# Optimization experiments

Measured on AMD Instinct MI355X. Metric: run time of the kernel, lower is better.

## Reference

```python
import jax, jax.numpy as jnp
import numpy as np

B, T, D, H = 8, 256, 1024, 512
NUM_SPANS = T * (T + 1) // 2          # triangular span enumeration
K = int(2.0 * T)                      # pruning_ratio * num_tokens
NUM_GOLD = 10
NEG = -1e20                           # allennlp replace_masked_values fill

# static triangular (start, end) index tables: for start in range(T): for end in range(start, T)
_starts = np.repeat(np.arange(T), np.arange(T, 0, -1))
_ends = np.concatenate([np.arange(s, T) for s in range(T)])
START_IDX = jnp.asarray(_starts, dtype=jnp.int32)
END_IDX = jnp.asarray(_ends, dtype=jnp.int32)


def setup_inputs() -> dict:
    key = jax.random.key(0)
    ks = jax.random.split(key, 8)
    inputs = jax.random.normal(ks[0], (B, T, D), dtype=jnp.float32)
    input_mask = jnp.ones((B, T), dtype=jnp.int32)
    # gold spans with start <= end, all in range (sorted along last dim)
    answer_spans = jnp.sort(jax.random.randint(ks[1], (B, NUM_GOLD, 2), 0, T), axis=-1)
    sD = 1.0 / np.sqrt(D)
    sH = 1.0 / np.sqrt(H)
    W_start = jax.random.uniform(ks[2], (D, H), jnp.float32, -sD, sD)
    b_start = jax.random.uniform(ks[3], (H,), jnp.float32, -sD, sD)
    W_end = jax.random.uniform(ks[4], (D, H), jnp.float32, -sD, sD)
    b_end = jax.random.uniform(ks[5], (H,), jnp.float32, -sD, sD)
    w_score = jax.random.uniform(ks[6], (H, 1), jnp.float32, -sH, sH)
    b_score = jax.random.uniform(ks[7], (1,), jnp.float32, -sH, sH)
    return {"inputs": inputs, "input_mask": input_mask, "answer_spans": answer_spans,
            "W_start": W_start, "b_start": b_start, "W_end": W_end, "b_end": b_end,
            "w_score": w_score, "b_score": b_score}


def reference(inputs, input_mask, answer_spans, W_start, b_start, W_end, b_end, w_score, b_score):
    # SpanRepAssembly: project starts/ends, pairwise-sum over triangular spans
    hs = inputs @ W_start + b_start                        # [B,T,H]
    he = inputs @ W_end + b_end                            # [B,T,H]
    span_hidden = hs[:, START_IDX, :] + he[:, END_IDX, :]  # [B,S,H]
    m = input_mask.astype(bool)
    span_mask = m[:, START_IDX] & m[:, END_IDX]            # [B,S]

    # span scorer: ReLU -> Linear(H,1)
    scores = jax.nn.relu(span_hidden) @ w_score + b_score  # [B,S,1]
    scores = jnp.where(span_mask[..., None], scores, NEG)

    # Pruner: top-k by score, indices sorted ascending, gather
    _, top_idx = jax.lax.top_k(scores[..., 0], K)          # [B,K]
    top_idx = jnp.sort(top_idx, axis=1)
    top_logits = jnp.take_along_axis(scores, top_idx[..., None], axis=1)       # [B,K,1]
    top_mask = jnp.take_along_axis(span_mask, top_idx, axis=1)[..., None].astype(jnp.float32)
    top_probs = jax.nn.sigmoid(top_logits) * top_mask

    # gold prediction map (union policy): labels[b, tri_index(span)] = 1
    s0 = answer_spans[..., 0].astype(jnp.int32)
    e0 = answer_spans[..., 1].astype(jnp.int32)
    gmask = (s0 >= 0)
    arg_idx = (2 * s0 * T - s0 * s0 + s0) // 2 + (e0 - s0)
    arg_idx = jnp.where(gmask, arg_idx, 0)
    labels = jnp.zeros((B, NUM_SPANS), jnp.float32)
    labels = labels.at[jnp.arange(B)[:, None], arg_idx].max(gmask.astype(jnp.float32))
    pred = jnp.take_along_axis(labels[..., None], top_idx[..., None], axis=1)  # [B,K,1]

    # BCE-with-logits, weight=top_mask, reduction='sum' (stable form)
    l = top_logits
    bce = jnp.maximum(l, 0.0) - l * pred + jnp.log1p(jnp.exp(-jnp.abs(l)))
    loss = jnp.sum(top_mask * bce)
    return top_probs, loss
```

## Files before the change

kernel.cpp:

```cpp
#include <hip/hip_runtime.h>
#include <hip/hip_bf16.h>
#include <math.h>

#define BB 8
#define TT 256
#define DD 1024
#define HH 512
#define NSPANS 32896
#define KK 512
#define NEGV -1e20f
#define NCH 32
#define CHSZ 1028
#define NT16 72

typedef __attribute__((ext_vector_type(8))) short bf16x8;
typedef __attribute__((ext_vector_type(4))) float f32x4;

__device__ inline unsigned short f2bf(float f) {
    unsigned u = __float_as_uint(f);
    return (unsigned short)((u + 0x7FFFu + ((u >> 16) & 1u)) >> 16);
}
__device__ inline float bf2f(unsigned short u) {
    return __uint_as_float(((unsigned)u) << 16);
}
__device__ inline void split3(float v, unsigned short& a, unsigned short& b,
                              unsigned short& c) {
    a = f2bf(v);           float r  = v - bf2f(a);
    b = f2bf(r);           float r2 = r - bf2f(b);
    c = f2bf(r2);
}

__global__ __launch_bounds__(256) void prep(
    const float* __restrict__ X,
    const float* __restrict__ Ws, const float* __restrict__ We,
    unsigned short* __restrict__ x0, unsigned short* __restrict__ x1,
    unsigned short* __restrict__ x2, unsigned short* __restrict__ wt,
    unsigned* __restrict__ zp)
{
    const int blk = blockIdx.x;
    const int tid = threadIdx.x;

    if (blk < 2048) {
        const int i4 = blk * 256 + tid;
        const float4 v = ((const float4*)X)[i4];
        const float vv[4] = {v.x, v.y, v.z, v.w};
        ushort4 h0, h1, h2;
        unsigned short* p0 = (unsigned short*)&h0;
        unsigned short* p1 = (unsigned short*)&h1;
        unsigned short* p2 = (unsigned short*)&h2;
        #pragma unroll
        for (int j = 0; j < 4; ++j) split3(vv[j], p0[j], p1[j], p2[j]);
        ((ushort4*)x0)[i4] = h0;
        ((ushort4*)x1)[i4] = h1;
        ((ushort4*)x2)[i4] = h2;
    } else if (blk < 3072) {
        __shared__ float lt[32][33];
        const int blk2 = blk - 2048;
        const int z   = blk2 >> 9;
        const int rem = blk2 & 511;
        const int k0  = (rem >> 4) * 32;
        const int h0  = (rem & 15) * 32;

        const float* Wz = z ? We : Ws;
        {
            const int row = tid >> 3, c4 = tid & 7;
            const float4 v = *(const float4*)&Wz[(k0 + row) * HH + h0 + c4 * 4];
            lt[row][c4*4 + 0] = v.x;
            lt[row][c4*4 + 1] = v.y;
            lt[row][c4*4 + 2] = v.z;
            lt[row][c4*4 + 3] = v.w;
        }
        __syncthreads();
        {
            const int n = h0 + (tid >> 3), kq = tid & 7;
            ushort4 o0, o1, o2;
            unsigned short* q0 = (unsigned short*)&o0;
            unsigned short* q1 = (unsigned short*)&o1;
            unsigned short* q2 = (unsigned short*)&o2;
            #pragma unroll
            for (int u = 0; u < 4; ++u)
                split3(lt[kq*4 + u][tid >> 3], q0[u], q1[u], q2[u]);
            unsigned short* base = wt + (size_t)z * 3 * 524288;
            const int off = n * 1024 + k0 + kq * 4;
            *(ushort4*)&base[0 * 524288 + off] = o0;
            *(ushort4*)&base[1 * 524288 + off] = o1;
            *(ushort4*)&base[2 * 524288 + off] = o2;
        }
    } else {
        const int i = (blk - 3072) * 256 + tid;
        for (int k = i; k < 32777; k += 32 * 256) zp[k] = 0u;
    }
}

__global__ __launch_bounds__(256) void gemm_mfma(
    const unsigned short* __restrict__ xs,
    const unsigned short* __restrict__ wt,
    const float* __restrict__ bs, const float* __restrict__ be,
    float* __restrict__ hs, float* __restrict__ he)
{
    const int bid = blockIdx.x;
    const int lg  = ((bid & 7) << 6) + (bid >> 3);
    const int z   = lg >> 8;
    const int my  = (lg & 255) >> 3, nx = lg & 7;
    const int m0 = my * 64, n0 = nx * 64;

    const unsigned short* __restrict__ W = wt + (size_t)z * 3 * 524288;
    const float* __restrict__ bias = z ? be : bs;
    float* __restrict__ Y = z ? he : hs;

    __shared__ __align__(16) unsigned short la[3][64][72];
    __shared__ __align__(16) unsigned short lb[3][64][72];

    const int tid = threadIdx.x;
    const int wave = tid >> 6, lane = tid & 63;
    const int wm = (wave >> 1) * 32, wn = (wave & 1) * 32;

    f32x4 acc[2][2];
    #pragma unroll
    for (int i = 0; i < 2; ++i)
        #pragma unroll
        for (int j = 0; j < 2; ++j) acc[i][j] = (f32x4){0.f, 0.f, 0.f, 0.f};

    const int rA = lane & 15;
    const int kq = lane >> 4;

    for (int kt = 0; kt < 16; ++kt) {
        const int k0 = kt * 64;
        __syncthreads();
        #pragma unroll
        for (int sp = 0; sp < 3; ++sp) {
            #pragma unroll
            for (int it = 0; it < 2; ++it) {
                const int idx = it * 256 + tid;
                const int row = idx >> 3, c8 = idx & 7;
                *(int4*)&la[sp][row][c8 * 8] =
                    *(const int4*)&xs[(size_t)sp * 2097152 + (m0 + row) * 1024 + k0 + c8 * 8];
                *(int4*)&lb[sp][row][c8 * 8] =
                    *(const int4*)&W[(size_t)sp * 524288 + (n0 + row) * 1024 + k0 + c8 * 8];
            }
        }
        __syncthreads();

        #pragma unroll
        for (int s = 0; s < 2; ++s) {
            const int kl = s * 32 + kq * 8;
            bf16x8 af[3][2], bg[3][2];
            #pragma unroll
            for (int sp = 0; sp < 3; ++sp) {
                #pragma unroll
                for (int f = 0; f < 2; ++f) {
                    af[sp][f] = *(const bf16x8*)&la[sp][wm + f * 16 + rA][kl];
                    bg[sp][f] = *(const bf16x8*)&lb[sp][wn + f * 16 + rA][kl];
                }
            }
            #pragma unroll
            for (int fm = 0; fm < 2; ++fm)
                #pragma unroll
                for (int fn = 0; fn < 2; ++fn) {
                    acc[fm][fn] = __builtin_amdgcn_mfma_f32_16x16x32_bf16(
                        af[0][fm], bg[0][fn], acc[fm][fn], 0, 0, 0);
                    acc[fm][fn] = __builtin_amdgcn_mfma_f32_16x16x32_bf16(
                        af[0][fm], bg[1][fn], acc[fm][fn], 0, 0, 0);
                    acc[fm][fn] = __builtin_amdgcn_mfma_f32_16x16x32_bf16(
                        af[1][fm], bg[0][fn], acc[fm][fn], 0, 0, 0);
                    acc[fm][fn] = __builtin_amdgcn_mfma_f32_16x16x32_bf16(
                        af[1][fm], bg[1][fn], acc[fm][fn], 0, 0, 0);
                    acc[fm][fn] = __builtin_amdgcn_mfma_f32_16x16x32_bf16(
                        af[0][fm], bg[2][fn], acc[fm][fn], 0, 0, 0);
                    acc[fm][fn] = __builtin_amdgcn_mfma_f32_16x16x32_bf16(
                        af[2][fm], bg[0][fn], acc[fm][fn], 0, 0, 0);
                }
        }
    }

    const int col = lane & 15, rq = lane >> 4;
    #pragma unroll
    for (int fm = 0; fm < 2; ++fm)
        #pragma unroll
        for (int fn = 0; fn < 2; ++fn) {
            const int nn = n0 + wn + fn * 16 + col;
            const float bv = bias[nn];
            #pragma unroll
            for (int r = 0; r < 4; ++r) {
                const int mm = m0 + wm + fm * 16 + rq * 4 + r;
                Y[mm * HH + nn] = acc[fm][fn][r] + bv;
            }
        }
}

__device__ inline unsigned f2key(float f) {
    unsigned u = __float_as_uint(f);
    return u ^ ((u & 0x80000000u) ? 0xFFFFFFFFu : 0x80000000u);
}

__global__ __launch_bounds__(128) void span_scores(
    const float* __restrict__ hs, const float* __restrict__ he,
    const float* __restrict__ w_score, const float* __restrict__ b_score,
    const int* __restrict__ input_mask, float* __restrict__ scores,
    unsigned* __restrict__ hist12)
{
    const int bx = blockIdx.x;
    const int b = bx / NT16;
    int tI = bx - b * NT16;
    int i = 0, cnt = 8;
    while (tI >= cnt) { tI -= cnt; ++i; cnt = 8 - (i >> 1); }
    const int j = (i >> 1) + tI;
    const int s0 = i * 16, e0 = j * 32;

    __shared__ __align__(16) float shs[16][132];
    __shared__ __align__(16) float she[32][132];
    __shared__ __align__(16) float swc[128];
    __shared__ unsigned lh[2048];

    const int tid = threadIdx.x;
    const float4* hs4 = (const float4*)hs;
    const float4* he4 = (const float4*)he;

    for (int idx = tid; idx < 2048; idx += 128) lh[idx] = 0;

    const int ii = tid >> 4, jj = tid & 15;

    float4 acc[2][2];
    #pragma unroll
    for (int p = 0; p < 2; ++p)
        #pragma unroll
        for (int q = 0; q < 2; ++q) acc[p][q] = make_float4(0.f, 0.f, 0.f, 0.f);

    for (int ck = 0; ck < 4; ++ck) {
        const int kc = ck * 128;
        __syncthreads();
        #pragma unroll
        for (int l = 0; l < 12; ++l) {
            const int idx = l * 128 + tid;
            const int row = idx >> 5, c4 = idx & 31;
            if (row < 16) {
                *(float4*)&shs[row][c4 * 4] =
                    hs4[((b*TT + s0 + row) * HH + kc) / 4 + c4];
            } else {
                *(float4*)&she[row - 16][c4 * 4] =
                    he4[((b*TT + e0 + row - 16) * HH + kc) / 4 + c4];
            }
        }
        if (tid < 32) *(float4*)&swc[tid * 4] =
            ((const float4*)w_score)[kc / 4 + tid];
        __syncthreads();

        #pragma unroll 4
        for (int c4 = 0; c4 < 32; ++c4) {
            const float4 w  = *(const float4*)&swc[c4 * 4];
            const float4 a0 = *(const float4*)&shs[ii][c4 * 4];
            const float4 a1 = *(const float4*)&shs[ii + 8][c4 * 4];
            const float4 v0 = *(const float4*)&she[jj][c4 * 4];
            const float4 v1 = *(const float4*)&she[jj + 16][c4 * 4];
            #pragma unroll
            for (int p = 0; p < 2; ++p) {
                const float4 a = p ? a1 : a0;
                #pragma unroll
                for (int q = 0; q < 2; ++q) {
                    const float4 v = q ? v1 : v0;
                    acc[p][q].x += fmaxf(a.x + v.x, 0.f) * w.x;
                    acc[p][q].y += fmaxf(a.y + v.y, 0.f) * w.y;
                    acc[p][q].z += fmaxf(a.z + v.z, 0.f) * w.z;
                    acc[p][q].w += fmaxf(a.w + v.w, 0.f) * w.w;
                }
            }
        }
    }

    const float bsc = b_score[0];
    #pragma unroll
    for (int p = 0; p < 2; ++p) {
        const int s = s0 + ii + p * 8;
        #pragma unroll
        for (int q = 0; q < 2; ++q) {
            const int e = e0 + jj + q * 16;
            if (e >= s) {
                const float4 a4 = acc[p][q];
                float scv = (a4.x + a4.y) + (a4.z + a4.w) + bsc;
                if (!(input_mask[b*TT + s] && input_mask[b*TT + e])) scv = NEGV;
                scores[b*NSPANS + s*TT - (s*(s-1))/2 + (e - s)] = scv;
                const unsigned bin = f2key(scv) >> 20;
                atomicAdd(&lh[bin >> 1], 1u << ((bin & 1u) * 16));
            }
        }
    }
    __syncthreads();

    for (int idx = tid; idx < 2048; idx += 128) {
        const unsigned w = lh[idx];
        const unsigned lo = w & 0xFFFFu, hi = w >> 16;
        if (lo) atomicAdd(&hist12[b*4096 + 2*idx],     lo);
        if (hi) atomicAdd(&hist12[b*4096 + 2*idx + 1], hi);
    }
}

__global__ __launch_bounds__(256) void findcompact(
    const float* __restrict__ scores, const unsigned* __restrict__ hist12,
    unsigned* __restrict__ thrInfo,
    unsigned* __restrict__ cand, unsigned* __restrict__ candCnt)
{
    const int b = blockIdx.x >> 5, ch = blockIdx.x & 31;
    const unsigned* h = hist12 + b * 4096;
    const int tid = threadIdx.x;
    const int lane = tid & 63, wave = tid >> 6;

    const int topbin = 4095 - tid * 16;
    unsigned psum = 0;
    #pragma unroll
    for (int j = 0; j < 16; ++j) psum += h[topbin - j];

    unsigned inc = psum;
    #pragma unroll
    for (int off = 1; off < 64; off <<= 1) {
        unsigned v = __shfl_up(inc, off);
        if (lane >= off) inc += v;
    }
    __shared__ unsigned wsum4[4], wpre4[4];
    __shared__ unsigned shp[2];
    if (lane == 63) wsum4[wave] = inc;
    __syncthreads();
    if (tid == 0) { unsigned c = 0; for (int w = 0; w < 4; ++w) { wpre4[w] = c; c += wsum4[w]; } }
    __syncthreads();

    const unsigned before = wpre4[wave] + inc - psum;
    if (before < KK && before + psum >= KK) {
        unsigned cum = before;
        int bin = topbin;
        #pragma unroll
        for (int j = 0; j < 16; ++j) {
            const unsigned c = h[topbin - j];
            if (cum + c >= KK) { bin = topbin - j; break; }
            cum += c;
        }
        shp[0] = (unsigned)bin;
        shp[1] = KK - cum;
        thrInfo[b*4 + 0] = (unsigned)bin;
        thrInfo[b*4 + 1] = KK - cum;
    }
    __syncthreads();
    const unsigned p12 = shp[0];

    const float* sc = scores + b * NSPANS;
    const int base = ch * CHSZ;
    for (int i = base + tid; i < base + CHSZ; i += 256) {
        const unsigned key = f2key(sc[i]);
        if ((key >> 20) == p12) {
            const unsigned pos = atomicAdd(&candCnt[b], 1u);
            cand[b*NSPANS + pos] = key & 0xFFFFFu;
        }
    }
}

__global__ __launch_bounds__(1024) void refine(
    const unsigned* __restrict__ cand, const unsigned* __restrict__ candCnt,
    const float* __restrict__ scores,
    unsigned* __restrict__ thrInfo, unsigned* __restrict__ chunkBase)
{
    const int b = blockIdx.x;
    const unsigned* cd = cand + b*NSPANS;
    const unsigned n = candCnt[b];
    const unsigned remaining = thrInfo[b*4 + 1];
    const int tid = threadIdx.x;
    const int lane = tid & 63, wave = tid >> 6;

    __shared__ unsigned hist[1024];
    __shared__ unsigned wsum[16], wpre[16];
    __shared__ unsigned sh[2], shT[2];

    hist[tid] = 0;
    __syncthreads();
    for (unsigned i = tid; i < n; i += 1024) atomicAdd(&hist[(cd[i] >> 10) & 1023u], 1u);
    __syncthreads();
    {
        const unsigned psum = hist[1023 - tid];
        unsigned inc = psum;
        #pragma unroll
        for (int off = 1; off < 64; off <<= 1) {
            unsigned v = __shfl_up(inc, off);
            if (lane >= off) inc += v;
        }
        if (lane == 63) wsum[wave] = inc;
        __syncthreads();
        if (tid == 0) { unsigned c = 0; for (int w = 0; w < 16; ++w) { wpre[w] = c; c += wsum[w]; } }
        __syncthreads();
        const unsigned before = wpre[wave] + inc - psum;
        if (before < remaining && before + psum >= remaining && psum > 0) {
            sh[0] = 1023u - (unsigned)tid;
            sh[1] = remaining - before;
        }
        __syncthreads();
    }
    const unsigned b1 = sh[0], rem1 = sh[1];
    __syncthreads();

    hist[tid] = 0;
    __syncthreads();
    for (unsigned i = tid; i < n; i += 1024) {
        const unsigned v = cd[i];
        if (((v >> 10) & 1023u) == b1) atomicAdd(&hist[v & 1023u], 1u);
    }
    __syncthreads();
    {
        const unsigned psum = hist[1023 - tid];
        unsigned inc = psum;
        #pragma unroll
        for (int off = 1; off < 64; off <<= 1) {
            unsigned v = __shfl_up(inc, off);
            if (lane >= off) inc += v;
        }
        if (lane == 63) wsum[wave] = inc;
        __syncthreads();
        if (tid == 0) { unsigned c = 0; for (int w = 0; w < 16; ++w) { wpre[w] = c; c += wsum[w]; } }
        __syncthreads();
        const unsigned before = wpre[wave] + inc - psum;
        if (before < rem1 && before + psum >= rem1 && psum > 0) {
            const unsigned thrv = (thrInfo[b*4 + 0] << 20) | (b1 << 10) | (1023u - (unsigned)tid);
            thrInfo[b*4 + 2] = thrv;
            thrInfo[b*4 + 3] = rem1 - before;
            shT[0] = thrv;
            shT[1] = rem1 - before;
        }
    }
    __syncthreads();
    const unsigned thr = shT[0], ties = shT[1];

    __shared__ unsigned cg[NCH], ce[NCH];
    const float* sc = scores + b*NSPANS;
    #pragma unroll
    for (int q = 0; q < 2; ++q) {
        const int ch = wave*2 + q;
        const int base = ch*CHSZ, end = base + CHSZ;
        unsigned g = 0, e = 0;
        for (int i = base + lane; i < end; i += 64) {
            const unsigned key = f2key(sc[i]);
            g += (key > thr); e += (key == thr);
        }
        #pragma unroll
        for (int off = 32; off; off >>= 1) { g += __shfl_down(g, off); e += __shfl_down(e, off); }
        if (lane == 0) { cg[ch] = g; ce[ch] = e; }
    }
    __syncthreads();

    if (tid == 0) {
        unsigned out = 0, eqp = 0;
        for (int c = 0; c < NCH; ++c) {
            chunkBase[(b*NCH + c)*2 + 0] = out;
            chunkBase[(b*NCH + c)*2 + 1] = eqp;
            const unsigned room = (eqp >= ties) ? 0u : (ties - eqp);
            const unsigned taken = (ce[c] < room) ? ce[c] : room;
            out += cg[c] + taken;
            eqp += ce[c];
        }
    }
}

__global__ __launch_bounds__(256) void scatter_final(
    const float* __restrict__ scores, const unsigned* __restrict__ thrInfo,
    const unsigned* __restrict__ chunkBase, const int* __restrict__ answer_spans,
    float* __restrict__ chunkLoss, unsigned* __restrict__ ticket,
    float* __restrict__ out)
{
    const int b = blockIdx.x >> 5, ch = blockIdx.x & 31;
    const float* sc = scores + b*NSPANS;
    const unsigned thr = thrInfo[b*4 + 2], ties = thrInfo[b*4 + 3];
    unsigned outPos = chunkBase[(b*NCH + ch)*2 + 0];
    unsigned eqPos  = chunkBase[(b*NCH + ch)*2 + 1];

    const int tid = threadIdx.x, wave = tid >> 6, lane = tid & 63;
    const unsigned long long lmask = (1ull << lane) - 1ull;
    __shared__ unsigned wS[4], wE[4];
    __shared__ int gold[10];
    __shared__ float wLoss[4];
    __shared__ unsigned lastFlag;

    if (tid < 10) {
        const int s0 = answer_spans[b*20 + tid*2];
        const int e0 = answer_spans[b*20 + tid*2 + 1];
        gold[tid] = (s0 >= 0) ? ((2*s0*TT - s0*s0 + s0)/2 + (e0 - s0)) : -1;
    }
    __syncthreads();

    float lsum = 0.f;
    const int base = ch*CHSZ;
    for (int seg = base; seg < base + CHSZ; seg += 256) {
        const int i = seg + tid;
        const bool valid = (i < base + CHSZ);
        const float v = valid ? sc[i] : 0.f;
        const unsigned key = valid ? f2key(v) : 0u;
        const bool g  = valid && key > thr;
        const bool eq = valid && key == thr;

        const unsigned long long meq = __ballot(eq);
        if (lane == 0) wE[wave] = (unsigned)__popcll(meq);
        __syncthreads();

        unsigned eqPre = eqPos;
        for (int w = 0; w < wave; ++w) eqPre += wE[w];
        const unsigned myEqRank = eqPre + (unsigned)__popcll(meq & lmask);
        const bool sel = g || (eq && myEqRank < ties);

        const unsigned long long msel = __ballot(sel);
        if (lane == 0) wS[wave] = (unsigned)__popcll(msel);
        __syncthreads();

        unsigned selPre = outPos;
        for (int w = 0; w < wave; ++w) selPre += wS[w];
        if (sel) {
            const unsigned pos = b*KK + selPre + (unsigned)__popcll(msel & lmask);
            float prob = 0.f;
            if (v > -1e19f) {
                prob = 1.f / (1.f + expf(-v));
                float pred = 0.f;
                #pragma unroll
                for (int gq = 0; gq < 10; ++gq)
                    if (gold[gq] == i) pred = 1.f;
                lsum += fmaxf(v, 0.f) - v*pred + log1pf(expf(-fabsf(v)));
            }
            out[pos] = prob;
        }

        unsigned totS = 0, totE = 0;
        #pragma unroll
        for (int w = 0; w < 4; ++w) { totS += wS[w]; totE += wE[w]; }
        __syncthreads();
        outPos += totS; eqPos += totE;
    }

    #pragma unroll
    for (int off = 32; off; off >>= 1) lsum += __shfl_down(lsum, off);
    if (lane == 0) wLoss[wave] = lsum;
    __syncthreads();
    if (tid == 0) {
        chunkLoss[b*NCH + ch] = (wLoss[0] + wLoss[1]) + (wLoss[2] + wLoss[3]);
        __threadfence();
        lastFlag = atomicAdd(ticket, 1u);
    }
    __syncthreads();

    if (lastFlag == BB*NCH - 1) {
        __threadfence();
        float cl = atomicAdd(&chunkLoss[tid], 0.f);
        #pragma unroll
        for (int off = 32; off; off >>= 1) cl += __shfl_down(cl, off);
        if (lane == 0) wLoss[wave] = cl;
        __syncthreads();
        if (tid == 0)
            out[BB*KK] = (wLoss[0] + wLoss[1]) + (wLoss[2] + wLoss[3]);
    }
}

extern "C" void kernel_launch(void* const* d_in, const int* in_sizes, int n_in,
                              void* d_out, int out_size, void* d_ws, size_t ws_size,
                              hipStream_t stream)
{
    const float* inputs       = (const float*)d_in[0];
    const int*   input_mask   = (const int*)  d_in[1];
    const int*   answer_spans = (const int*)  d_in[2];
    const float* W_start      = (const float*)d_in[3];
    const float* b_start      = (const float*)d_in[4];
    const float* W_end        = (const float*)d_in[5];
    const float* b_end        = (const float*)d_in[6];
    const float* w_score      = (const float*)d_in[7];
    const float* b_score      = (const float*)d_in[8];
    float* out = (float*)d_out;
    unsigned* ws = (unsigned*)d_ws;

    float*    hs       = (float*)(ws);
    float*    he       = (float*)(ws + 1048576);
    float*    scores   = (float*)(ws + 2097152);
    unsigned* thrInfo  = ws + 2364416;
    unsigned* chunkBase= ws + 2364448;
    unsigned* hist12   = ws + 2364960;
    unsigned* candCnt  = ws + 2397728;
    unsigned* ticket   = ws + 2397736;
    unsigned short* xs = (unsigned short*)(ws + 2397740);
    unsigned short* wt = (unsigned short*)(ws + 5543468);
    float*    chunkLoss= (float*)(ws + 8689196);
    unsigned* cand     = (unsigned*)hs;

    prep<<<3104, 256, 0, stream>>>(inputs, W_start, W_end,
                                   xs, xs + 2097152, xs + 4194304, wt, hist12);

    gemm_mfma<<<512, 256, 0, stream>>>(xs, wt, b_start, b_end, hs, he);

    span_scores<<<BB*NT16, 128, 0, stream>>>(hs, he, w_score, b_score, input_mask,
                                             scores, hist12);

    findcompact  <<<BB*NCH, 256, 0, stream>>>(scores, hist12, thrInfo, cand, candCnt);
    refine       <<<BB, 1024, 0, stream>>>(cand, candCnt, scores, thrInfo, chunkBase);
    scatter_final<<<BB*NCH, 256, 0, stream>>>(scores, thrInfo, chunkBase,
                                              answer_spans, chunkLoss, ticket, out);
}
```

Baseline: 115.2 us.

## Use 128x128 GEMM tiles with split-K halves and register prefetch

The bf16x3 GEMM now uses 128x128 output tiles with a 4x4 MFMA fragment per wave, which raises operand reuse per LDS load. K is split into two halves, each written to its own partial buffer, so the grid stays at 256 blocks. The next K slice is prefetched into registers while the current one is computed. span_scores sums the two partial buffers when loading, which doubles its hs/he read traffic, and the larger accumulator set raises register pressure.

```diff
diff --git a/kernel.cpp b/kernel.cpp
--- a/kernel.cpp
+++ b/kernel.cpp
@@ -96,90 +96,106 @@
     const unsigned short* __restrict__ xs,
     const unsigned short* __restrict__ wt,
     const float* __restrict__ bs, const float* __restrict__ be,
-    float* __restrict__ hs, float* __restrict__ he)
+    float* __restrict__ hs_lo, float* __restrict__ hs_hi,
+    float* __restrict__ he_lo, float* __restrict__ he_hi)
 {
     const int bid = blockIdx.x;
-    const int lg  = ((bid & 7) << 6) + (bid >> 3);
-    const int z   = lg >> 8;
-    const int my  = (lg & 255) >> 3, nx = lg & 7;
-    const int m0 = my * 64, n0 = nx * 64;
+    const int lg  = ((bid & 7) << 5) + (bid >> 3);
+    const int z   = lg >> 7;
+    const int kh  = (lg >> 6) & 1;
+    const int my  = (lg & 63) >> 2;
+    const int nx  = lg & 3;
+    const int m0 = my * 128, n0 = nx * 128, kb = kh * 512;
 
     const unsigned short* __restrict__ W = wt + (size_t)z * 3 * 524288;
     const float* __restrict__ bias = z ? be : bs;
-    float* __restrict__ Y = z ? he : hs;
-
-    __shared__ __align__(16) unsigned short la[3][64][72];
-    __shared__ __align__(16) unsigned short lb[3][64][72];
+    float* __restrict__ Y = z ? (kh ? he_hi : he_lo) : (kh ? hs_hi : hs_lo);
+
+    __shared__ __align__(16) unsigned short la[3][128][40];
+    __shared__ __align__(16) unsigned short lb[3][128][40];
 
     const int tid = threadIdx.x;
     const int wave = tid >> 6, lane = tid & 63;
-    const int wm = (wave >> 1) * 32, wn = (wave & 1) * 32;
-
-    f32x4 acc[2][2];
-    #pragma unroll
-    for (int i = 0; i < 2; ++i)
-        #pragma unroll
-        for (int j = 0; j < 2; ++j) acc[i][j] = (f32x4){0.f, 0.f, 0.f, 0.f};
-
-    const int rA = lane & 15;
-    const int kq = lane >> 4;
+    const int wm = (wave >> 1) * 64, wn = (wave & 1) * 64;
+    const int rA = lane & 15, kq = lane >> 4;
+
+    f32x4 acc[4][4];
+    #pragma unroll
+    for (int i = 0; i < 4; ++i)
+        #pragma unroll
+        for (int j = 0; j < 4; ++j) acc[i][j] = (f32x4){0.f, 0.f, 0.f, 0.f};
+
+    int4 pa[3][2], pb[3][2];
+    const int lrow = tid >> 2, lc8 = tid & 3;
+    const int lrow2 = (256 + tid) >> 2, lc82 = tid & 3;
+
+    #pragma unroll
+    for (int sp = 0; sp < 3; ++sp) {
+        pa[sp][0] = *(const int4*)&xs[(size_t)sp*2097152 + (m0+lrow )*1024 + kb + lc8 *8];
+        pa[sp][1] = *(const int4*)&xs[(size_t)sp*2097152 + (m0+lrow2)*1024 + kb + lc82*8];
+        pb[sp][0] = *(const int4*)&W [(size_t)sp*524288  + (n0+lrow )*1024 + kb + lc8 *8];
+        pb[sp][1] = *(const int4*)&W [(size_t)sp*524288  + (n0+lrow2)*1024 + kb + lc82*8];
+    }
 
     for (int kt = 0; kt < 16; ++kt) {
-        const int k0 = kt * 64;
         __syncthreads();
         #pragma unroll
         for (int sp = 0; sp < 3; ++sp) {
-            #pragma unroll
-            for (int it = 0; it < 2; ++it) {
-                const int idx = it * 256 + tid;
-                const int row = idx >> 3, c8 = idx & 7;
-                *(int4*)&la[sp][row][c8 * 8] =
-                    *(const int4*)&xs[(size_t)sp * 2097152 + (m0 + row) * 1024 + k0 + c8 * 8];
-                *(int4*)&lb[sp][row][c8 * 8] =
-                    *(const int4*)&W[(size_t)sp * 524288 + (n0 + row) * 1024 + k0 + c8 * 8];
-            }
-        }
-        __syncthreads();
-
-        #pragma unroll
-        for (int s = 0; s < 2; ++s) {
-            const int kl = s * 32 + kq * 8;
-            bf16x8 af[3][2], bg[3][2];
+            *(int4*)&la[sp][lrow ][lc8 *8] = pa[sp][0];
+            *(int4*)&la[sp][lrow2][lc82*8] = pa[sp][1];
+            *(int4*)&lb[sp][lrow ][lc8 *8] = pb[sp][0];
+            *(int4*)&lb[sp][lrow2][lc82*8] = pb[sp][1];
+        }
+        __syncthreads();
+
+        if (kt < 15) {
+            const int k0n = kb + (kt + 1) * 32;
             #pragma unroll
             for (int sp = 0; sp < 3; ++sp) {
-                #pragma unroll
-                for (int f = 0; f < 2; ++f) {
-                    af[sp][f] = *(const bf16x8*)&la[sp][wm + f * 16 + rA][kl];
-                    bg[sp][f] = *(const bf16x8*)&lb[sp][wn + f * 16 + rA][kl];
-                }
+                pa[sp][0] = *(const int4*)&xs[(size_t)sp*2097152 + (m0+lrow )*1024 + k0n + lc8 *8];
+                pa[sp][1] = *(const int4*)&xs[(size_t)sp*2097152 + (m0+lrow2)*1024 + k0n + lc82*8];
+                pb[sp][0] = *(const int4*)&W [(size_t)sp*524288  + (n0+lrow )*1024 + k0n + lc8 *8];
+                pb[sp][1] = *(const int4*)&W [(size_t)sp*524288  + (n0+lrow2)*1024 + k0n + lc82*8];
             }
+        }
+
+        bf16x8 bg[3][4];
+        #pragma unroll
+        for (int sp = 0; sp < 3; ++sp)
             #pragma unroll
-            for (int fm = 0; fm < 2; ++fm)
-                #pragma unroll
-                for (int fn = 0; fn < 2; ++fn) {
-                    acc[fm][fn] = __builtin_amdgcn_mfma_f32_16x16x32_bf16(
-                        af[0][fm], bg[0][fn], acc[fm][fn], 0, 0, 0);
-                    acc[fm][fn] = __builtin_amdgcn_mfma_f32_16x16x32_bf16(
-                        af[0][fm], bg[1][fn], acc[fm][fn], 0, 0, 0);
-                    acc[fm][fn] = __builtin_amdgcn_mfma_f32_16x16x32_bf16(
-                        af[1][fm], bg[0][fn], acc[fm][fn], 0, 0, 0);
-                    acc[fm][fn] = __builtin_amdgcn_mfma_f32_16x16x32_bf16(
-                        af[1][fm], bg[1][fn], acc[fm][fn], 0, 0, 0);
-                    acc[fm][fn] = __builtin_amdgcn_mfma_f32_16x16x32_bf16(
-                        af[0][fm], bg[2][fn], acc[fm][fn], 0, 0, 0);
-                    acc[fm][fn] = __builtin_amdgcn_mfma_f32_16x16x32_bf16(
-                        af[2][fm], bg[0][fn], acc[fm][fn], 0, 0, 0);
-                }
+            for (int fn = 0; fn < 4; ++fn)
+                bg[sp][fn] = *(const bf16x8*)&lb[sp][wn + fn*16 + rA][kq*8];
+
+        #pragma unroll
+        for (int fm = 0; fm < 4; ++fm) {
+            bf16x8 af0 = *(const bf16x8*)&la[0][wm + fm*16 + rA][kq*8];
+            bf16x8 af1 = *(const bf16x8*)&la[1][wm + fm*16 + rA][kq*8];
+            bf16x8 af2 = *(const bf16x8*)&la[2][wm + fm*16 + rA][kq*8];
+            #pragma unroll
+            for (int fn = 0; fn < 4; ++fn) {
+                acc[fm][fn] = __builtin_amdgcn_mfma_f32_16x16x32_bf16(
+                    af0, bg[0][fn], acc[fm][fn], 0, 0, 0);
+                acc[fm][fn] = __builtin_amdgcn_mfma_f32_16x16x32_bf16(
+                    af0, bg[1][fn], acc[fm][fn], 0, 0, 0);
+                acc[fm][fn] = __builtin_amdgcn_mfma_f32_16x16x32_bf16(
+                    af1, bg[0][fn], acc[fm][fn], 0, 0, 0);
+                acc[fm][fn] = __builtin_amdgcn_mfma_f32_16x16x32_bf16(
+                    af1, bg[1][fn], acc[fm][fn], 0, 0, 0);
+                acc[fm][fn] = __builtin_amdgcn_mfma_f32_16x16x32_bf16(
+                    af0, bg[2][fn], acc[fm][fn], 0, 0, 0);
+                acc[fm][fn] = __builtin_amdgcn_mfma_f32_16x16x32_bf16(
+                    af2, bg[0][fn], acc[fm][fn], 0, 0, 0);
+            }
         }
     }
 
     const int col = lane & 15, rq = lane >> 4;
     #pragma unroll
-    for (int fm = 0; fm < 2; ++fm)
-        #pragma unroll
-        for (int fn = 0; fn < 2; ++fn) {
+    for (int fm = 0; fm < 4; ++fm)
+        #pragma unroll
+        for (int fn = 0; fn < 4; ++fn) {
             const int nn = n0 + wn + fn * 16 + col;
-            const float bv = bias[nn];
+            const float bv = kh ? 0.f : bias[nn];
             #pragma unroll
             for (int r = 0; r < 4; ++r) {
                 const int mm = m0 + wm + fm * 16 + rq * 4 + r;
@@ -194,7 +210,8 @@
 }
 
 __global__ __launch_bounds__(128) void span_scores(
-    const float* __restrict__ hs, const float* __restrict__ he,
+    const float* __restrict__ hs_lo, const float* __restrict__ hs_hi,
+    const float* __restrict__ he_lo, const float* __restrict__ he_hi,
     const float* __restrict__ w_score, const float* __restrict__ b_score,
     const int* __restrict__ input_mask, float* __restrict__ scores,
     unsigned* __restrict__ hist12)
@@ -213,8 +230,10 @@
     __shared__ unsigned lh[2048];
 
     const int tid = threadIdx.x;
-    const float4* hs4 = (const float4*)hs;
-    const float4* he4 = (const float4*)he;
+    const float4* hsl4 = (const float4*)hs_lo;
+    const float4* hsh4 = (const float4*)hs_hi;
+    const float4* hel4 = (const float4*)he_lo;
+    const float4* heh4 = (const float4*)he_hi;
 
     for (int idx = tid; idx < 2048; idx += 128) lh[idx] = 0;
 
@@ -234,11 +253,19 @@
             const int idx = l * 128 + tid;
             const int row = idx >> 5, c4 = idx & 31;
             if (row < 16) {
-                *(float4*)&shs[row][c4 * 4] =
-                    hs4[((b*TT + s0 + row) * HH + kc) / 4 + c4];
+                const int off = ((b*TT + s0 + row) * HH + kc) / 4 + c4;
+                const float4 a = hsl4[off], bsum = hsh4[off];
+                float4 s4;
+                s4.x = a.x + bsum.x; s4.y = a.y + bsum.y;
+                s4.z = a.z + bsum.z; s4.w = a.w + bsum.w;
+                *(float4*)&shs[row][c4 * 4] = s4;
             } else {
-                *(float4*)&she[row - 16][c4 * 4] =
-                    he4[((b*TT + e0 + row - 16) * HH + kc) / 4 + c4];
+                const int off = ((b*TT + e0 + row - 16) * HH + kc) / 4 + c4;
+                const float4 a = hel4[off], bsum = heh4[off];
+                float4 s4;
+                s4.x = a.x + bsum.x; s4.y = a.y + bsum.y;
+                s4.z = a.z + bsum.z; s4.w = a.w + bsum.w;
+                *(float4*)&she[row - 16][c4 * 4] = s4;
             }
         }
         if (tid < 32) *(float4*)&swc[tid * 4] =
@@ -565,25 +592,29 @@
     float* out = (float*)d_out;
     unsigned* ws = (unsigned*)d_ws;
 
-    float*    hs       = (float*)(ws);
-    float*    he       = (float*)(ws + 1048576);
-    float*    scores   = (float*)(ws + 2097152);
-    unsigned* thrInfo  = ws + 2364416;
-    unsigned* chunkBase= ws + 2364448;
-    unsigned* hist12   = ws + 2364960;
-    unsigned* candCnt  = ws + 2397728;
-    unsigned* ticket   = ws + 2397736;
-    unsigned short* xs = (unsigned short*)(ws + 2397740);
-    unsigned short* wt = (unsigned short*)(ws + 5543468);
-    float*    chunkLoss= (float*)(ws + 8689196);
-    unsigned* cand     = (unsigned*)hs;
+    float*    hs_lo    = (float*)(ws);
+    float*    he_lo    = (float*)(ws + 1048576);
+    float*    hs_hi    = (float*)(ws + 2097152);
+    float*    he_hi    = (float*)(ws + 3145728);
+    float*    scores   = (float*)(ws + 4194304);
+    unsigned* thrInfo  = ws + 4457472;
+    unsigned* chunkBase= ws + 4457504;
+    unsigned* hist12   = ws + 4458016;
+    unsigned* candCnt  = ws + 4490784;
+    unsigned* ticket   = ws + 4490792;
+    float*    chunkLoss= (float*)(ws + 4490796);
+    unsigned short* xs = (unsigned short*)(ws + 4491056);
+    unsigned short* wt = (unsigned short*)(ws + 7636784);
+    unsigned* cand     = (unsigned*)hs_lo;
 
     prep<<<3104, 256, 0, stream>>>(inputs, W_start, W_end,
                                    xs, xs + 2097152, xs + 4194304, wt, hist12);
 
-    gemm_mfma<<<512, 256, 0, stream>>>(xs, wt, b_start, b_end, hs, he);
-
-    span_scores<<<BB*NT16, 128, 0, stream>>>(hs, he, w_score, b_score, input_mask,
+    gemm_mfma<<<256, 256, 0, stream>>>(xs, wt, b_start, b_end,
+                                       hs_lo, hs_hi, he_lo, he_hi);
+
+    span_scores<<<BB*NT16, 128, 0, stream>>>(hs_lo, hs_hi, he_lo, he_hi,
+                                             w_score, b_score, input_mask,
                                              scores, hist12);
 
     findcompact  <<<BB*NCH, 256, 0, stream>>>(scores, hist12, thrInfo, cand, candCnt);
```

Result: slower. 162.8 us (+41.3%).
